# Kernel optimization log

Measured on AMD Instinct MI355X. Metric: run time of the kernel, lower is better.

The kernel has to match this reference:

```python
import jax, jax.numpy as jnp
import numpy as np

N_NODES = 100000
N_EDGES = 500000
D = 128


def setup_inputs() -> dict:
    key = jax.random.key(0)
    ks = jax.random.split(key, 6)
    x = jax.random.normal(ks[0], (N_NODES, D), dtype=jnp.float32)
    edge_index = jax.random.randint(ks[1], (2, N_EDGES), 0, N_NODES, dtype=jnp.int64)
    edge_label = jax.random.randint(ks[2], (N_EDGES,), 0, 2, dtype=jnp.int64)
    # MLP params (dim_in -> dim_in, 2 layers, has_act=True, has_bias=True)
    scale = 1.0 / np.sqrt(D)
    W1 = jax.random.normal(ks[3], (D, D), dtype=jnp.float32) * scale
    b1 = jnp.zeros((D,), dtype=jnp.float32)
    W2 = jax.random.normal(ks[4], (D, D), dtype=jnp.float32) * scale
    b2 = jnp.zeros((D,), dtype=jnp.float32)
    return {"x": x, "edge_index": edge_index, "edge_label": edge_label,
            "W1": W1, "b1": b1, "W2": W2, "b2": b2}


def reference(x, edge_index, edge_label, W1, b1, W2, b2):
    # post-MP MLP on all node features (has_act=True -> ReLU after each layer)
    h = jax.nn.relu(x @ W1 + b1)          # [N, D]
    h = jax.nn.relu(h @ W2 + b2)          # [N, D]
    # gather endpoints: batch.x[edge_index] -> [2, E, D]
    v1 = h[edge_index[0]]                  # [E, D]
    v2 = h[edge_index[1]]                  # [E, D]
    # dot decode: sum(v1 * v2, dim=-1)
    pred = jnp.sum(v1 * v2, axis=-1)       # [E]
    return pred, edge_label
```

## Files before the change

kernel.cpp:

```cpp
#include <hip/hip_runtime.h>

typedef __attribute__((ext_vector_type(8))) short short8;
typedef __attribute__((ext_vector_type(4))) short short4v;
typedef __attribute__((ext_vector_type(4))) float floatx4;

#define D 128
#define NWAVES 4
#define GRID_MLP 512

__device__ __forceinline__ unsigned short f2bf(float f) {
  unsigned u = __float_as_uint(f);
  u += 0x7FFFu + ((u >> 16) & 1u);
  return (unsigned short)(u >> 16);
}

__device__ __forceinline__ void stageW(const float* __restrict__ W,
                                       unsigned short* __restrict__ sW, int tid) {
  const int n = tid & 127;
  const int tg = tid >> 7;
  #pragma unroll
  for (int iter = 0; iter < 16; ++iter) {
    const int k0 = iter * 8 + tg * 4;
    float w0 = W[(k0 + 0) * D + n];
    float w1 = W[(k0 + 1) * D + n];
    float w2 = W[(k0 + 2) * D + n];
    float w3 = W[(k0 + 3) * D + n];
    short4v p;
    p[0] = (short)f2bf(w0); p[1] = (short)f2bf(w1);
    p[2] = (short)f2bf(w2); p[3] = (short)f2bf(w3);
    const int idx = n * D + (((k0 >> 3) ^ (n & 15)) << 3) + (k0 & 7);
    *(short4v*)&sW[idx] = p;
  }
}


__global__ __launch_bounds__(256) void mlp_layer1(
    const float* __restrict__ x, const float* __restrict__ W1,
    const float* __restrict__ b1, unsigned short* __restrict__ h,
    int nNodes, int ntiles) {
  __shared__ unsigned short sW[D * D];
  __shared__ unsigned short sH[NWAVES][16 * D];
  const int tid = threadIdx.x;
  const int wave = tid >> 6, lane = tid & 63;
  const int quad = lane >> 4, l16 = lane & 15;

  stageW(W1, sW, tid);
  __syncthreads();

  float bias[8];
  #pragma unroll
  for (int n0 = 0; n0 < 8; ++n0) bias[n0] = b1[n0 * 16 + l16];

  unsigned short* mysH = sH[wave];

  for (int t = blockIdx.x * NWAVES + wave; t < ntiles; t += GRID_MLP * NWAVES) {
    const int m = t * 16 + l16;
    const bool mv = (m < nNodes);
    float4 xf[8];
    const float* xp = x + (size_t)m * D + quad * 8;
    #pragma unroll
    for (int kk = 0; kk < 4; ++kk) {
      if (mv) {
        xf[2 * kk]     = *(const float4*)(xp + kk * 32);
        xf[2 * kk + 1] = *(const float4*)(xp + kk * 32 + 4);
      } else {
        xf[2 * kk] = make_float4(0, 0, 0, 0);
        xf[2 * kk + 1] = make_float4(0, 0, 0, 0);
      }
    }
    floatx4 acc[8];
    #pragma unroll
    for (int n0 = 0; n0 < 8; ++n0) acc[n0] = (floatx4){0.f, 0.f, 0.f, 0.f};
    #pragma unroll
    for (int kk = 0; kk < 4; ++kk) {
      const float4 f0 = xf[2 * kk], f1 = xf[2 * kk + 1];
      short8 a;
      a[0] = (short)f2bf(f0.x); a[1] = (short)f2bf(f0.y);
      a[2] = (short)f2bf(f0.z); a[3] = (short)f2bf(f0.w);
      a[4] = (short)f2bf(f1.x); a[5] = (short)f2bf(f1.y);
      a[6] = (short)f2bf(f1.z); a[7] = (short)f2bf(f1.w);
      #pragma unroll
      for (int n0 = 0; n0 < 8; ++n0) {
        short8 b = *(const short8*)&sW[(n0 * 16 + l16) * D + (((kk * 4 + quad) ^ l16) << 3)];
        acc[n0] = __builtin_amdgcn_mfma_f32_16x16x32_bf16(a, b, acc[n0], 0, 0, 0);
      }
    }
    #pragma unroll
    for (int n0 = 0; n0 < 8; ++n0) {
      #pragma unroll
      for (int r = 0; r < 4; ++r) {
        float v = acc[n0][r] + bias[n0];
        v = v > 0.f ? v : 0.f;
        const int row = quad * 4 + r;
        const int g = 2 * n0 + (l16 >> 3);
        mysH[row * D + (((g ^ row) & 15) << 3) + (l16 & 7)] = f2bf(v);
      }
    }
    #pragma unroll
    for (int i = 0; i < 4; ++i) {
      const int row = i * 4 + quad;
      short8 vrow = *(const short8*)&mysH[row * D + (((l16 ^ row) & 15) << 3)];
      const int g = t * 16 + row;
      if (g < nNodes) *(short8*)&h[(size_t)g * D + l16 * 8] = vrow;
    }
  }
}

__global__ __launch_bounds__(256) void mlp_layer2(
    unsigned short* __restrict__ h, const float* __restrict__ W2,
    const float* __restrict__ b2, int nNodes, int ntiles) {
  __shared__ unsigned short sW[D * D];
  __shared__ unsigned short sH[NWAVES][16 * D];
  const int tid = threadIdx.x;
  const int wave = tid >> 6, lane = tid & 63;
  const int quad = lane >> 4, l16 = lane & 15;

  stageW(W2, sW, tid);
  __syncthreads();

  float bias[8];
  #pragma unroll
  for (int n0 = 0; n0 < 8; ++n0) bias[n0] = b2[n0 * 16 + l16];

  unsigned short* mysH = sH[wave];

  for (int t = blockIdx.x * NWAVES + wave; t < ntiles; t += GRID_MLP * NWAVES) {
    const int m = t * 16 + l16;
    const bool mv = (m < nNodes);
    short8 af[4];
    #pragma unroll
    for (int kk = 0; kk < 4; ++kk) {
      if (mv) af[kk] = *(const short8*)&h[(size_t)m * D + kk * 32 + quad * 8];
      else    af[kk] = (short8){0, 0, 0, 0, 0, 0, 0, 0};
    }
    floatx4 acc[8];
    #pragma unroll
    for (int n0 = 0; n0 < 8; ++n0) acc[n0] = (floatx4){0.f, 0.f, 0.f, 0.f};
    #pragma unroll
    for (int kk = 0; kk < 4; ++kk) {
      #pragma unroll
      for (int n0 = 0; n0 < 8; ++n0) {
        short8 b = *(const short8*)&sW[(n0 * 16 + l16) * D + (((kk * 4 + quad) ^ l16) << 3)];
        acc[n0] = __builtin_amdgcn_mfma_f32_16x16x32_bf16(af[kk], b, acc[n0], 0, 0, 0);
      }
    }
    #pragma unroll
    for (int n0 = 0; n0 < 8; ++n0) {
      #pragma unroll
      for (int r = 0; r < 4; ++r) {
        float v = acc[n0][r] + bias[n0];
        v = v > 0.f ? v : 0.f;
        const int row = quad * 4 + r;
        const int g = 2 * n0 + (l16 >> 3);
        mysH[row * D + (((g ^ row) & 15) << 3) + (l16 & 7)] = f2bf(v);
      }
    }
    #pragma unroll
    for (int i = 0; i < 4; ++i) {
      const int row = i * 4 + quad;
      short8 vrow = *(const short8*)&mysH[row * D + (((l16 ^ row) & 15) << 3)];
      const int g = t * 16 + row;
      if (g < nNodes) *(short8*)&h[(size_t)g * D + l16 * 8] = vrow;
    }
  }
}

__device__ __forceinline__ float dot2bf(unsigned a, unsigned b, float acc) {
  float a0 = __uint_as_float(a << 16);
  float a1 = __uint_as_float(a & 0xFFFF0000u);
  float b0 = __uint_as_float(b << 16);
  float b1 = __uint_as_float(b & 0xFFFF0000u);
  acc = fmaf(a0, b0, acc);
  acc = fmaf(a1, b1, acc);
  return acc;
}

__global__ __launch_bounds__(256) void edge_kernel(
    const unsigned short* __restrict__ h2, const int* __restrict__ eidx,
    const int* __restrict__ elabel, float* __restrict__ out, int E) {
  const int sub = threadIdx.x & 15;
  const int grp = (blockIdx.x * 256 + threadIdx.x) >> 4;
  const int e0 = grp * 4;
  uint4 va[4], vb[4];
  #pragma unroll
  for (int i = 0; i < 4; ++i) {
    const int e = e0 + i;
    if (e < E) {
      const int s = eidx[e];
      const int d = eidx[E + e];
      va[i] = *(const uint4*)(h2 + (size_t)s * D + sub * 8);
      vb[i] = *(const uint4*)(h2 + (size_t)d * D + sub * 8);
    }
  }
  #pragma unroll
  for (int i = 0; i < 4; ++i) {
    const int e = e0 + i;
    if (e < E) {
      float acc = 0.f;
      acc = dot2bf(va[i].x, vb[i].x, acc);
      acc = dot2bf(va[i].y, vb[i].y, acc);
      acc = dot2bf(va[i].z, vb[i].z, acc);
      acc = dot2bf(va[i].w, vb[i].w, acc);
      acc += __shfl_xor(acc, 8);
      acc += __shfl_xor(acc, 4);
      acc += __shfl_xor(acc, 2);
      acc += __shfl_xor(acc, 1);
      if (sub == 0) out[e] = acc;
    }
  }
  for (int le = blockIdx.x * 256 + threadIdx.x; le < E; le += gridDim.x * 256)
    out[E + le] = (float)elabel[le];
}

extern "C" void kernel_launch(void* const* d_in, const int* in_sizes, int n_in,
                              void* d_out, int out_size, void* d_ws, size_t ws_size,
                              hipStream_t stream) {
  const float* x  = (const float*)d_in[0];
  const int* eidx = (const int*)d_in[1];
  const int* elab = (const int*)d_in[2];
  const float* W1 = (const float*)d_in[3];
  const float* b1 = (const float*)d_in[4];
  const float* W2 = (const float*)d_in[5];
  const float* b2 = (const float*)d_in[6];
  float* out = (float*)d_out;

  const int nNodes = in_sizes[0] / D;
  const int E = in_sizes[2];
  const int ntiles = (nNodes + 15) / 16;

  unsigned short* h = (unsigned short*)d_ws;

  mlp_layer1<<<GRID_MLP, 256, 0, stream>>>(x, W1, b1, h, nNodes, ntiles);
  mlp_layer2<<<GRID_MLP, 256, 0, stream>>>(h, W2, b2, nNodes, ntiles);

  const int edgeBlocks = (E + 63) / 64;
  edge_kernel<<<edgeBlocks, 256, 0, stream>>>(h, eidx, elab, out, E);
}
```

Before: 147.6 us.

## Fuse both MLP layers into one kernel and batch edge gathers per group

Merges the two MLP layer kernels into one kernel. The layer-1 output tile stays in shared memory and feeds layer 2 directly, so the intermediate h is no longer written to and read back from global memory. The label copy moves into the MLP kernel. The edge kernel now handles 8 edges per 16-lane group with vectorized index loads, giving more loads in flight. The cost is double the shared memory for weights (two 32KB bf16 matrices), which may lower occupancy, plus more registers in the edge kernel.

Result: faster. 140.5 us (-4.8%).

```diff
diff --git a/kernel.cpp b/kernel.cpp
--- a/kernel.cpp
+++ b/kernel.cpp
@@ -33,23 +33,29 @@
   }
 }
 
-
-__global__ __launch_bounds__(256) void mlp_layer1(
+__global__ __launch_bounds__(256) void mlp_fused(
     const float* __restrict__ x, const float* __restrict__ W1,
-    const float* __restrict__ b1, unsigned short* __restrict__ h,
-    int nNodes, int ntiles) {
-  __shared__ unsigned short sW[D * D];
+    const float* __restrict__ b1, const float* __restrict__ W2,
+    const float* __restrict__ b2, unsigned short* __restrict__ h,
+    const int* __restrict__ elabel, float* __restrict__ out,
+    int nNodes, int ntiles, int E) {
+  __shared__ unsigned short sW1[D * D];
+  __shared__ unsigned short sW2[D * D];
   __shared__ unsigned short sH[NWAVES][16 * D];
   const int tid = threadIdx.x;
   const int wave = tid >> 6, lane = tid & 63;
   const int quad = lane >> 4, l16 = lane & 15;
 
-  stageW(W1, sW, tid);
+  for (int le = blockIdx.x * 256 + tid; le < E; le += GRID_MLP * 256)
+    out[E + le] = (float)elabel[le];
+
+  stageW(W1, sW1, tid);
+  stageW(W2, sW2, tid);
   __syncthreads();
 
-  float bias[8];
+  float bias1[8], bias2[8];
   #pragma unroll
-  for (int n0 = 0; n0 < 8; ++n0) bias[n0] = b1[n0 * 16 + l16];
+  for (int n0 = 0; n0 < 8; ++n0) { bias1[n0] = b1[n0 * 16 + l16]; bias2[n0] = b2[n0 * 16 + l16]; }
 
   unsigned short* mysH = sH[wave];
 
@@ -81,7 +87,7 @@
       a[6] = (short)f2bf(f1.z); a[7] = (short)f2bf(f1.w);
       #pragma unroll
       for (int n0 = 0; n0 < 8; ++n0) {
-        short8 b = *(const short8*)&sW[(n0 * 16 + l16) * D + (((kk * 4 + quad) ^ l16) << 3)];
+        short8 b = *(const short8*)&sW1[(n0 * 16 + l16) * D + (((kk * 4 + quad) ^ l16) << 3)];
         acc[n0] = __builtin_amdgcn_mfma_f32_16x16x32_bf16(a, b, acc[n0], 0, 0, 0);
       }
     }
@@ -89,58 +95,24 @@
     for (int n0 = 0; n0 < 8; ++n0) {
       #pragma unroll
       for (int r = 0; r < 4; ++r) {
-        float v = acc[n0][r] + bias[n0];
+        float v = acc[n0][r] + bias1[n0];
         v = v > 0.f ? v : 0.f;
         const int row = quad * 4 + r;
         const int g = 2 * n0 + (l16 >> 3);
         mysH[row * D + (((g ^ row) & 15) << 3) + (l16 & 7)] = f2bf(v);
       }
     }
-    #pragma unroll
-    for (int i = 0; i < 4; ++i) {
-      const int row = i * 4 + quad;
-      short8 vrow = *(const short8*)&mysH[row * D + (((l16 ^ row) & 15) << 3)];
-      const int g = t * 16 + row;
-      if (g < nNodes) *(short8*)&h[(size_t)g * D + l16 * 8] = vrow;
-    }
-  }
-}
-
-__global__ __launch_bounds__(256) void mlp_layer2(
-    unsigned short* __restrict__ h, const float* __restrict__ W2,
-    const float* __restrict__ b2, int nNodes, int ntiles) {
-  __shared__ unsigned short sW[D * D];
-  __shared__ unsigned short sH[NWAVES][16 * D];
-  const int tid = threadIdx.x;
-  const int wave = tid >> 6, lane = tid & 63;
-  const int quad = lane >> 4, l16 = lane & 15;
-
-  stageW(W2, sW, tid);
-  __syncthreads();
-
-  float bias[8];
-  #pragma unroll
-  for (int n0 = 0; n0 < 8; ++n0) bias[n0] = b2[n0 * 16 + l16];
-
-  unsigned short* mysH = sH[wave];
-
-  for (int t = blockIdx.x * NWAVES + wave; t < ntiles; t += GRID_MLP * NWAVES) {
-    const int m = t * 16 + l16;
-    const bool mv = (m < nNodes);
     short8 af[4];
     #pragma unroll
+    for (int kk = 0; kk < 4; ++kk)
+      af[kk] = *(const short8*)&mysH[l16 * D + ((((kk * 4 + quad) ^ l16) & 15) << 3)];
+    #pragma unroll
+    for (int n0 = 0; n0 < 8; ++n0) acc[n0] = (floatx4){0.f, 0.f, 0.f, 0.f};
+    #pragma unroll
     for (int kk = 0; kk < 4; ++kk) {
-      if (mv) af[kk] = *(const short8*)&h[(size_t)m * D + kk * 32 + quad * 8];
-      else    af[kk] = (short8){0, 0, 0, 0, 0, 0, 0, 0};
-    }
-    floatx4 acc[8];
-    #pragma unroll
-    for (int n0 = 0; n0 < 8; ++n0) acc[n0] = (floatx4){0.f, 0.f, 0.f, 0.f};
-    #pragma unroll
-    for (int kk = 0; kk < 4; ++kk) {
       #pragma unroll
       for (int n0 = 0; n0 < 8; ++n0) {
-        short8 b = *(const short8*)&sW[(n0 * 16 + l16) * D + (((kk * 4 + quad) ^ l16) << 3)];
+        short8 b = *(const short8*)&sW2[(n0 * 16 + l16) * D + (((kk * 4 + quad) ^ l16) << 3)];
         acc[n0] = __builtin_amdgcn_mfma_f32_16x16x32_bf16(af[kk], b, acc[n0], 0, 0, 0);
       }
     }
@@ -148,7 +120,7 @@
     for (int n0 = 0; n0 < 8; ++n0) {
       #pragma unroll
       for (int r = 0; r < 4; ++r) {
-        float v = acc[n0][r] + bias[n0];
+        float v = acc[n0][r] + bias2[n0];
         v = v > 0.f ? v : 0.f;
         const int row = quad * 4 + r;
         const int g = 2 * n0 + (l16 >> 3);
@@ -175,41 +147,53 @@
   return acc;
 }
 
+__device__ __forceinline__ float edge_dot(const uint4& a, const uint4& b) {
+  float acc = 0.f;
+  acc = dot2bf(a.x, b.x, acc);
+  acc = dot2bf(a.y, b.y, acc);
+  acc = dot2bf(a.z, b.z, acc);
+  acc = dot2bf(a.w, b.w, acc);
+  acc += __shfl_xor(acc, 8);
+  acc += __shfl_xor(acc, 4);
+  acc += __shfl_xor(acc, 2);
+  acc += __shfl_xor(acc, 1);
+  return acc;
+}
+
 __global__ __launch_bounds__(256) void edge_kernel(
     const unsigned short* __restrict__ h2, const int* __restrict__ eidx,
-    const int* __restrict__ elabel, float* __restrict__ out, int E) {
+    float* __restrict__ out, int E) {
   const int sub = threadIdx.x & 15;
   const int grp = (blockIdx.x * 256 + threadIdx.x) >> 4;
-  const int e0 = grp * 4;
-  uint4 va[4], vb[4];
-  #pragma unroll
-  for (int i = 0; i < 4; ++i) {
-    const int e = e0 + i;
-    if (e < E) {
+  const int e0 = grp * 8;
+  if (e0 + 8 <= E) {
+    const int4 s0 = *(const int4*)&eidx[e0];
+    const int4 s1 = *(const int4*)&eidx[e0 + 4];
+    const int4 t0 = *(const int4*)&eidx[E + e0];
+    const int4 t1 = *(const int4*)&eidx[E + e0 + 4];
+    int s[8] = {s0.x, s0.y, s0.z, s0.w, s1.x, s1.y, s1.z, s1.w};
+    int d[8] = {t0.x, t0.y, t0.z, t0.w, t1.x, t1.y, t1.z, t1.w};
+    uint4 va[8], vb[8];
+    #pragma unroll
+    for (int i = 0; i < 8; ++i) {
+      va[i] = *(const uint4*)(h2 + (size_t)s[i] * D + sub * 8);
+      vb[i] = *(const uint4*)(h2 + (size_t)d[i] * D + sub * 8);
+    }
+    #pragma unroll
+    for (int i = 0; i < 8; ++i) {
+      float acc = edge_dot(va[i], vb[i]);
+      if (sub == 0) out[e0 + i] = acc;
+    }
+  } else if (e0 < E) {
+    for (int e = e0; e < E; ++e) {
       const int s = eidx[e];
       const int d = eidx[E + e];
-      va[i] = *(const uint4*)(h2 + (size_t)s * D + sub * 8);
-      vb[i] = *(const uint4*)(h2 + (size_t)d * D + sub * 8);
+      const uint4 ua = *(const uint4*)(h2 + (size_t)s * D + sub * 8);
+      const uint4 ub = *(const uint4*)(h2 + (size_t)d * D + sub * 8);
+      float acc = edge_dot(ua, ub);
+      if (sub == 0) out[e] = acc;
     }
   }
-  #pragma unroll
-  for (int i = 0; i < 4; ++i) {
-    const int e = e0 + i;
-    if (e < E) {
-      float acc = 0.f;
-      acc = dot2bf(va[i].x, vb[i].x, acc);
-      acc = dot2bf(va[i].y, vb[i].y, acc);
-      acc = dot2bf(va[i].z, vb[i].z, acc);
-      acc = dot2bf(va[i].w, vb[i].w, acc);
-      acc += __shfl_xor(acc, 8);
-      acc += __shfl_xor(acc, 4);
-      acc += __shfl_xor(acc, 2);
-      acc += __shfl_xor(acc, 1);
-      if (sub == 0) out[e] = acc;
-    }
-  }
-  for (int le = blockIdx.x * 256 + threadIdx.x; le < E; le += gridDim.x * 256)
-    out[E + le] = (float)elabel[le];
 }
 
 extern "C" void kernel_launch(void* const* d_in, const int* in_sizes, int n_in,
@@ -230,9 +214,9 @@
 
   unsigned short* h = (unsigned short*)d_ws;
 
-  mlp_layer1<<<GRID_MLP, 256, 0, stream>>>(x, W1, b1, h, nNodes, ntiles);
-  mlp_layer2<<<GRID_MLP, 256, 0, stream>>>(h, W2, b2, nNodes, ntiles);
-
-  const int edgeBlocks = (E + 63) / 64;
-  edge_kernel<<<edgeBlocks, 256, 0, stream>>>(h, eidx, elab, out, E);
-}
+  mlp_fused<<<GRID_MLP, 256, 0, stream>>>(x, W1, b1, W2, b2, h, elab, out,
+                                          nNodes, ntiles, E);
+
+  const int edgeBlocks = (E + 127) / 128;
+  edge_kernel<<<edgeBlocks, 256, 0, stream>>>(h, eidx, out, E);
+}
```
